# Kernel tuning notes

Measured on AMD Instinct MI355X. Metric: run time of the kernel, lower is better.

The kernel has to match this reference:

```python
import jax, jax.numpy as jnp
import numpy as np

B, N, D, H, HID, EN = 2, 4096, 128, 4, 32, 16
ALPHA = 0.2           # LeakyReLU slope
NEG = -9e15           # masked_fill value from the original code


def setup_inputs() -> dict:
    key = jax.random.key(0)
    ks = jax.random.split(key, 6)
    fea = jax.random.normal(ks[0], (B, N, D), dtype=jnp.float32)
    # binary dense adjacency (regulon x gene), square here so narrow() is identity
    adj = jax.random.randint(ks[1], (B, N, N), 0, 2).astype(jnp.float32)
    # per-head GAT params (xavier-ish scale)
    W_heads = jax.random.normal(ks[2], (H, D, HID), dtype=jnp.float32) * 0.1
    a_heads = jax.random.normal(ks[3], (H, 2 * HID, 1), dtype=jnp.float32) * 0.1
    W_last = jax.random.normal(ks[4], (H * HID, EN), dtype=jnp.float32) * 0.1
    a_last = jax.random.normal(ks[5], (2 * EN, 1), dtype=jnp.float32) * 0.1
    return {"fea_mats": fea, "adj_mats": adj, "W_heads": W_heads,
            "a_heads": a_heads, "W_last": W_last, "a_last": a_last}


def _gat_layer(x, adj, W, a, concat):
    # x: [N, d_in], adj: [nr, N], W: [d_in, out], a: [2*out, 1]
    out_dim = W.shape[1]
    wh = x @ W                                   # [N, out]
    nr = adj.shape[0]
    wh1 = wh[:nr] @ a[:out_dim]                  # [nr, 1]
    wh2 = wh @ a[out_dim:]                       # [N, 1]
    e = jax.nn.leaky_relu(wh1 + wh2.T, ALPHA)    # [nr, N]
    # _prepare_attentions: mask by adj, weight by adj, fill zeros with -9e15
    att = jnp.where(adj != 0, e * adj, 0.0)
    att = jnp.where(att == 0, NEG, att)
    att = jax.nn.softmax(att, axis=1)
    # the original detaches attention via a numpy roundtrip
    att = jax.lax.stop_gradient(att)
    res = att @ wh                               # [nr, out]
    return jax.nn.elu(res) if concat else res


def reference(fea_mats, adj_mats, W_heads, a_heads, W_last, a_last):
    def per_sample(x, adj):
        # multi-head attention layers (concat=True), vmapped over heads
        heads = jax.vmap(lambda W, a: _gat_layer(x, adj, W, a, True))(W_heads, a_heads)  # [H, N, HID]
        xcat = jnp.transpose(heads, (1, 0, 2)).reshape(x.shape[0], H * HID)  # torch.cat(dim=1)
        nr = adj.shape[0]
        out = _gat_layer(xcat, adj[:, :nr], W_last, a_last, False)  # adj.narrow(1,0,nr)
        return jax.nn.elu(out)  # [N, EN]
    return jax.vmap(per_sample)(fea_mats, adj_mats)  # [B, N, EN]
```

## Files before the change

### kernel.cpp

```cpp
#include <hip/hip_runtime.h>
#include <hip/hip_bf16.h>
#include <stdint.h>

#define B_ 2
#define N_ 4096
#define D_ 128
#define H_ 4
#define HID_ 32
#define EN_ 16
#define ALPHA_ 0.2f

typedef __attribute__((ext_vector_type(8))) short bf16x8;
typedef __attribute__((ext_vector_type(4))) float f32x4;
typedef __attribute__((ext_vector_type(8))) unsigned short u16x8;

__device__ __forceinline__ float bf2f(unsigned short u) {
    return __uint_as_float(((unsigned int)u) << 16);
}
__device__ __forceinline__ unsigned short f2bf_rne(float x) {
    unsigned int u = __float_as_uint(x);
    unsigned int r = ((u >> 16) & 1u) + 0x7fffu;
    return (unsigned short)((u + r) >> 16);
}
__device__ __forceinline__ unsigned int f2key(float x) {
    unsigned int u = __float_as_uint(x);
    return (u & 0x80000000u) ? ~u : (u | 0x80000000u);
}
__device__ __forceinline__ float key2f(unsigned int k) {
    unsigned int u = (k & 0x80000000u) ? (k ^ 0x80000000u) : ~k;
    return __uint_as_float(u);
}

__global__ __launch_bounds__(64) void zero_kernel(unsigned int* mk) {
    if (threadIdx.x < 16) mk[threadIdx.x] = 0u;
}

__global__ __launch_bounds__(256) void proj1_kernel(
    const float* __restrict__ fea, const float* __restrict__ Wh,
    float* __restrict__ wh)
{
    __shared__ float Ws[D_ * HID_];
    __shared__ float xs[8][D_];
    const int b = blockIdx.z, h = blockIdx.y;
    const int i0 = blockIdx.x * 8;
    const int tid = threadIdx.x;
    const float* Wp = Wh + h * D_ * HID_;
    for (int idx = tid * 4; idx < D_ * HID_; idx += 1024)
        *(float4*)&Ws[idx] = *(const float4*)(Wp + idx);
    const float* xp = fea + ((size_t)b * N_ + i0) * D_;
    *(float4*)&xs[(tid * 4) >> 7][(tid * 4) & 127] = *(const float4*)(xp + tid * 4);
    __syncthreads();
    const int r = tid >> 5, d = tid & 31;
    float acc = 0.f;
#pragma unroll 8
    for (int k = 0; k < D_; ++k) acc += xs[r][k] * Ws[k * HID_ + d];
    wh[(((size_t)b * H_ + h) * N_ + i0 + r) * HID_ + d] = acc;
}

__global__ __launch_bounds__(128) void proj1b_kernel(
    const float* __restrict__ wh, const float* __restrict__ a_heads,
    float* __restrict__ wh1, float* __restrict__ wh2,
    unsigned int* __restrict__ mkey, unsigned short* __restrict__ whTt)
{
    __shared__ float as_[2 * HID_];
    __shared__ unsigned short ts[32][136];
    const int b = blockIdx.z, h = blockIdx.y, tid = threadIdx.x;
    const int i = blockIdx.x * 128 + tid;
    if (tid < 2 * HID_) as_[tid] = a_heads[h * 2 * HID_ + tid];
    __syncthreads();
    const float* row = wh + (((size_t)b * H_ + h) * N_ + i) * HID_;
    float rv[32];
#pragma unroll
    for (int q = 0; q < 8; ++q) *(float4*)&rv[q * 4] = ((const float4*)row)[q];
    float a1 = 0.f, a2 = 0.f;
#pragma unroll
    for (int d = 0; d < HID_; ++d) {
        float v = rv[d];
        a1 += v * as_[d]; a2 += v * as_[HID_ + d];
        ts[d][tid] = f2bf_rne(v);
    }
    const size_t o = (size_t)(b * H_ + h) * N_ + i;
    wh1[o] = a1; wh2[o] = a2;
    float m = a2;
#pragma unroll
    for (int off = 32; off; off >>= 1) m = fmaxf(m, __shfl_xor(m, off));
    if ((tid & 63) == 0) atomicMax(&mkey[b * H_ + h], f2key(m));
    __syncthreads();
    const size_t base = ((size_t)(b * H_ + h) * 64 + blockIdx.x * 2) * 2048;
#pragma unroll
    for (int r = 0; r < 4; ++r) {
        int l = r * 128 + tid;
        int jb = l >> 8, d = (l >> 3) & 31, part = l & 7;
        *(u16x8*)(whTt + base + (size_t)jb * 2048 + d * 64 + part * 8) =
            *(const u16x8*)&ts[d][jb * 64 + part * 8];
    }
}

__global__ __launch_bounds__(256) void attn1_kernel(
    const float* __restrict__ adj, const unsigned short* __restrict__ whT,
    const float* __restrict__ wh1, const float* __restrict__ wh2,
    const unsigned int* __restrict__ mkey, float* __restrict__ x2)
{
    __shared__ float adj_s[2][16][68];
    __shared__ unsigned short whT_s[2][4][32][72];
    __shared__ float wh2_s[2][H_][64];
    __shared__ float lred[4][16];
    const int b = blockIdx.y, i0 = blockIdx.x * 16;
    const int tid = threadIdx.x, lane = tid & 63, h = tid >> 6;
    const int m = lane & 15, quad = lane >> 4;
    const float w1r = wh1[(size_t)(b * H_ + h) * N_ + i0 + m];
    const float Mh = key2f(mkey[b * H_ + h]);
    const float sb = w1r + Mh;
    const float mr = sb > 0.f ? sb : ALPHA_ * sb;
    const float* adjb = adj + ((size_t)b * N_ + i0) * N_;
    const float* wh2h = wh2 + (size_t)(b * H_ + h) * N_;
    const unsigned short* whTh = whT + (size_t)(b * H_ + h) * 64 * 2048;
    f32x4 acc0 = {0.f, 0.f, 0.f, 0.f}, acc1 = {0.f, 0.f, 0.f, 0.f};
    float lsum = 0.f;
    const int sr = tid >> 4, sc4 = (tid & 15) * 4;

    auto stage = [&](int jt, int buf) {
        *(float4*)&adj_s[buf][sr][sc4] = *(const float4*)(adjb + (size_t)sr * N_ + jt + sc4);
        wh2_s[buf][h][lane] = wh2h[jt + lane];
        const unsigned short* src = whTh + ((size_t)(jt >> 6)) * 2048;
#pragma unroll
        for (int r = 0; r < 4; ++r) {
            int l = r * 64 + lane;
            int d = l >> 3, part = l & 7;
            *(u16x8*)&whT_s[buf][h][d][part * 8] = *(const u16x8*)(src + l * 8);
        }
    };
    auto compute = [&](int buf) {
#pragma unroll
        for (int ks = 0; ks < 2; ++ks) {
            const int ko = ks * 32 + quad * 8;
            float a[8], w[8];
            *(float4*)&a[0] = *(const float4*)&adj_s[buf][m][ko];
            *(float4*)&a[4] = *(const float4*)&adj_s[buf][m][ko + 4];
            *(float4*)&w[0] = *(const float4*)&wh2_s[buf][h][ko];
            *(float4*)&w[4] = *(const float4*)&wh2_s[buf][h][ko + 4];
            bf16x8 af;
#pragma unroll
            for (int jj = 0; jj < 8; ++jj) {
                float s = w1r + w[jj];
                float e = s > 0.f ? s : ALPHA_ * s;
                float sc = e * a[jj];
                float p = (a[jj] != 0.f && sc != 0.f) ? __expf(sc - mr) : 0.f;
                unsigned short pb = f2bf_rne(p);
                af[jj] = (short)pb;
                lsum += bf2f(pb);
            }
            bf16x8 b0 = *(const bf16x8*)&whT_s[buf][h][m][ko];
            bf16x8 b1 = *(const bf16x8*)&whT_s[buf][h][m + 16][ko];
            acc0 = __builtin_amdgcn_mfma_f32_16x16x32_bf16(af, b0, acc0, 0, 0, 0);
            acc1 = __builtin_amdgcn_mfma_f32_16x16x32_bf16(af, b1, acc1, 0, 0, 0);
        }
    };

    stage(0, 0);
    int buf = 0;
    for (int jt = 0; jt < N_; jt += 64) {
        __syncthreads();
        if (jt + 64 < N_) stage(jt + 64, buf ^ 1);
        compute(buf);
        buf ^= 1;
    }
    lsum += __shfl_xor(lsum, 16);
    lsum += __shfl_xor(lsum, 32);
    if (lane < 16) lred[h][lane] = lsum;
    __syncthreads();
    float* obase = x2 + ((size_t)b * N_ + i0) * (H_ * HID_) + h * HID_;
#pragma unroll
    for (int reg = 0; reg < 4; ++reg) {
        int row = quad * 4 + reg;
        float linv = 1.f / fmaxf(lred[h][row], 1e-30f);
        float v0 = acc0[reg] * linv;
        float v1 = acc1[reg] * linv;
        v0 = v0 > 0.f ? v0 : expm1f(v0);
        v1 = v1 > 0.f ? v1 : expm1f(v1);
        obase[(size_t)row * (H_ * HID_) + m] = v0;
        obase[(size_t)row * (H_ * HID_) + 16 + m] = v1;
    }
}

__global__ __launch_bounds__(256) void proj2_kernel(
    const float* __restrict__ x2, const float* __restrict__ Wl,
    float* __restrict__ whl2)
{
    __shared__ float Ws[D_ * EN_];
    __shared__ float xs[16][D_];
    const int b = blockIdx.y, i0 = blockIdx.x * 16, tid = threadIdx.x;
    for (int idx = tid * 4; idx < D_ * EN_; idx += 1024)
        *(float4*)&Ws[idx] = *(const float4*)(Wl + idx);
    const float* xp = x2 + ((size_t)b * N_ + i0) * D_;
    for (int idx = tid * 4; idx < 16 * D_; idx += 1024)
        *(float4*)&xs[idx >> 7][idx & 127] = *(const float4*)(xp + idx);
    __syncthreads();
    const int r = tid >> 4, e = tid & 15;
    float acc = 0.f;
#pragma unroll 8
    for (int k = 0; k < D_; ++k) acc += xs[r][k] * Ws[k * EN_ + e];
    whl2[((size_t)b * N_ + i0 + r) * EN_ + e] = acc;
}

__global__ __launch_bounds__(128) void proj2b_kernel(
    const float* __restrict__ whl2, const float* __restrict__ a_last,
    float* __restrict__ wh1b, float* __restrict__ wh2b,
    unsigned int* __restrict__ mkey2, unsigned short* __restrict__ whT2t)
{
    __shared__ float as_[2 * EN_];
    __shared__ unsigned short ts[16][136];
    const int b = blockIdx.y, tid = threadIdx.x;
    const int i = blockIdx.x * 128 + tid;
    if (tid < 2 * EN_) as_[tid] = a_last[tid];
    __syncthreads();
    const float* row = whl2 + ((size_t)b * N_ + i) * EN_;
    float rv[16];
#pragma unroll
    for (int q = 0; q < 4; ++q) *(float4*)&rv[q * 4] = ((const float4*)row)[q];
    float a1 = 0.f, a2 = 0.f;
#pragma unroll
    for (int e = 0; e < EN_; ++e) {
        float v = rv[e];
        a1 += v * as_[e]; a2 += v * as_[EN_ + e];
        ts[e][tid] = f2bf_rne(v);
    }
    wh1b[(size_t)b * N_ + i] = a1; wh2b[(size_t)b * N_ + i] = a2;
    float m = a2;
#pragma unroll
    for (int off = 32; off; off >>= 1) m = fmaxf(m, __shfl_xor(m, off));
    if ((tid & 63) == 0) atomicMax(mkey2 + b, f2key(m));
    __syncthreads();
    const size_t base = ((size_t)b * 64 + blockIdx.x * 2) * 1024;
#pragma unroll
    for (int r = 0; r < 2; ++r) {
        int l = r * 128 + tid;
        int jb = l >> 7, d = (l >> 3) & 15, part = l & 7;
        *(u16x8*)(whT2t + base + (size_t)jb * 1024 + d * 64 + part * 8) =
            *(const u16x8*)&ts[d][jb * 64 + part * 8];
    }
}

__global__ __launch_bounds__(256) void attn2_kernel(
    const float* __restrict__ adj, const unsigned short* __restrict__ whT2,
    const float* __restrict__ wh1b, const float* __restrict__ wh2b,
    const unsigned int* __restrict__ mkey2, float* __restrict__ out)
{
    __shared__ float adj_s[2][16][268];
    __shared__ unsigned short wT_s[2][16][264];
    __shared__ float w2_s[2][256];
    __shared__ float accred[4][16][17];
    __shared__ float lredp[4][16];
    const int b = blockIdx.y, i0 = blockIdx.x * 16;
    const int tid = threadIdx.x, lane = tid & 63, w = tid >> 6;
    const int m = lane & 15, quad = lane >> 4;
    const float w1r = wh1b[(size_t)b * N_ + i0 + m];
    const float Mh = key2f(mkey2[b]);
    const float sb = w1r + Mh;
    const float mr = sb > 0.f ? sb : ALPHA_ * sb;
    const float* adjb = adj + ((size_t)b * N_ + i0) * N_;
    const float* w2g = wh2b + (size_t)b * N_;
    const unsigned short* wTg = whT2 + (size_t)b * 64 * 1024;
    f32x4 acc = {0.f, 0.f, 0.f, 0.f};
    float lsum = 0.f;
    const int sr = tid >> 4, sc = (tid & 15) * 4;

    auto stage = [&](int jt, int buf) {
#pragma unroll
        for (int r = 0; r < 4; ++r)
            *(float4*)&adj_s[buf][sr][r * 64 + sc] =
                *(const float4*)(adjb + (size_t)sr * N_ + jt + r * 64 + sc);
        w2_s[buf][tid] = w2g[jt + tid];
#pragma unroll
        for (int r = 0; r < 2; ++r) {
            int l = r * 256 + tid;
            int jb = l >> 7, t = l & 127;
            int d = t >> 3, part = t & 7;
            *(u16x8*)&wT_s[buf][d][jb * 64 + part * 8] =
                *(const u16x8*)(wTg + ((size_t)(jt >> 6) + jb) * 1024 + d * 64 + part * 8);
        }
    };
    auto compute = [&](int buf) {
#pragma unroll
        for (int ks = 0; ks < 2; ++ks) {
            const int ko = w * 64 + ks * 32 + quad * 8;
            float a[8], ww[8];
            *(float4*)&a[0] = *(const float4*)&adj_s[buf][m][ko];
            *(float4*)&a[4] = *(const float4*)&adj_s[buf][m][ko + 4];
            *(float4*)&ww[0] = *(const float4*)&w2_s[buf][ko];
            *(float4*)&ww[4] = *(const float4*)&w2_s[buf][ko + 4];
            bf16x8 af;
#pragma unroll
            for (int jj = 0; jj < 8; ++jj) {
                float s = w1r + ww[jj];
                float e = s > 0.f ? s : ALPHA_ * s;
                float sc2 = e * a[jj];
                float p = (a[jj] != 0.f && sc2 != 0.f) ? __expf(sc2 - mr) : 0.f;
                unsigned short pb = f2bf_rne(p);
                af[jj] = (short)pb;
                lsum += bf2f(pb);
            }
            bf16x8 bfr = *(const bf16x8*)&wT_s[buf][m][ko];
            acc = __builtin_amdgcn_mfma_f32_16x16x32_bf16(af, bfr, acc, 0, 0, 0);
        }
    };

    stage(0, 0);
    int buf = 0;
    for (int jt = 0; jt < N_; jt += 256) {
        __syncthreads();
        if (jt + 256 < N_) stage(jt + 256, buf ^ 1);
        compute(buf);
        buf ^= 1;
    }
    lsum += __shfl_xor(lsum, 16);
    lsum += __shfl_xor(lsum, 32);
    if (lane < 16) lredp[w][lane] = lsum;
#pragma unroll
    for (int reg = 0; reg < 4; ++reg)
        accred[w][quad * 4 + reg][m] = acc[reg];
    __syncthreads();
    const int row = tid >> 4, col = tid & 15;
    float s = accred[0][row][col] + accred[1][row][col]
            + accred[2][row][col] + accred[3][row][col];
    float l = lredp[0][row] + lredp[1][row] + lredp[2][row] + lredp[3][row];
    float v = s / fmaxf(l, 1e-30f);
    out[((size_t)b * N_ + i0 + row) * EN_ + col] = v > 0.f ? v : expm1f(v);
}

extern "C" void kernel_launch(void* const* d_in, const int* in_sizes, int n_in,
                              void* d_out, int out_size, void* d_ws, size_t ws_size,
                              hipStream_t stream)
{
    const float* fea = (const float*)d_in[0];
    const float* adj = (const float*)d_in[1];
    const float* Wh  = (const float*)d_in[2];
    const float* ah  = (const float*)d_in[3];
    const float* Wl  = (const float*)d_in[4];
    const float* al  = (const float*)d_in[5];

    float* ws   = (float*)d_ws;
    float* wh   = ws;
    float* wh1  = wh  + (size_t)B_ * H_ * N_ * HID_;
    float* wh2  = wh1 + (size_t)B_ * H_ * N_;
    float* x2   = wh2 + (size_t)B_ * H_ * N_;
    float* whl2 = x2  + (size_t)B_ * N_ * D_;
    float* wh1b = whl2 + (size_t)B_ * N_ * EN_;
    float* wh2b = wh1b + (size_t)B_ * N_;
    unsigned int* mkey = (unsigned int*)(wh2b + (size_t)B_ * N_);
    unsigned short* whTt  = (unsigned short*)(mkey + 16);
    unsigned short* whT2t = whTt + (size_t)B_ * H_ * 64 * 2048;

    zero_kernel<<<1, 64, 0, stream>>>(mkey);
    proj1_kernel<<<dim3(N_ / 8, H_, B_), 256, 0, stream>>>(fea, Wh, wh);
    proj1b_kernel<<<dim3(N_ / 128, H_, B_), 128, 0, stream>>>(wh, ah, wh1, wh2, mkey, whTt);
    attn1_kernel<<<dim3(N_ / 16, B_), 256, 0, stream>>>(adj, whTt, wh1, wh2, mkey, x2);
    proj2_kernel<<<dim3(N_ / 16, B_), 256, 0, stream>>>(x2, Wl, whl2);
    proj2b_kernel<<<dim3(N_ / 128, B_), 128, 0, stream>>>(whl2, al, wh1b, wh2b, mkey + 8, whT2t);
    attn2_kernel<<<dim3(N_ / 16, B_), 256, 0, stream>>>(adj, whT2t, wh1b, wh2b, mkey + 8,
                                                        (float*)d_out);
}
```

Baseline: 341.6 us.

## Split attention over key dimension with atomic accumulation and fused heads

Both attention kernels now split the key (j) dimension across S blocks and accumulate partial numerators and softmax denominators with float atomics. The normalisation and ELU are deferred to proj2 and a new finalize kernel. attn1 now processes all four heads per wave, reading the adjacency row once instead of staging it through shared memory. The exponent is moved to exp2 by pre-scaling the logits with log2(e). The change removes LDS double-buffering, adds a memset and many atomics, and makes results order-nondeterministic. It also changes the masking semantics slightly: sc!=0 becomes s!=0, and e*adj is treated as e for binary adjacency.

```diff
diff --git a/kernel.cpp b/kernel.cpp
--- a/kernel.cpp
+++ b/kernel.cpp
@@ -9,6 +9,9 @@
 #define HID_ 32
 #define EN_ 16
 #define ALPHA_ 0.2f
+#define S1_ 8
+#define S2_ 8
+#define LOG2E_ 1.4426950408889634f
 
 typedef __attribute__((ext_vector_type(8))) short bf16x8;
 typedef __attribute__((ext_vector_type(4))) float f32x4;
@@ -29,10 +32,6 @@
 __device__ __forceinline__ float key2f(unsigned int k) {
     unsigned int u = (k & 0x80000000u) ? (k ^ 0x80000000u) : ~k;
     return __uint_as_float(u);
-}
-
-__global__ __launch_bounds__(64) void zero_kernel(unsigned int* mk) {
-    if (threadIdx.x < 16) mk[threadIdx.x] = 0u;
 }
 
 __global__ __launch_bounds__(256) void proj1_kernel(
@@ -79,6 +78,7 @@
         a1 += v * as_[d]; a2 += v * as_[HID_ + d];
         ts[d][tid] = f2bf_rne(v);
     }
+    a1 *= LOG2E_; a2 *= LOG2E_;
     const size_t o = (size_t)(b * H_ + h) * N_ + i;
     wh1[o] = a1; wh2[o] = a2;
     float m = a2;
@@ -99,102 +99,106 @@
 __global__ __launch_bounds__(256) void attn1_kernel(
     const float* __restrict__ adj, const unsigned short* __restrict__ whT,
     const float* __restrict__ wh1, const float* __restrict__ wh2,
-    const unsigned int* __restrict__ mkey, float* __restrict__ x2)
-{
-    __shared__ float adj_s[2][16][68];
-    __shared__ unsigned short whT_s[2][4][32][72];
-    __shared__ float wh2_s[2][H_][64];
-    __shared__ float lred[4][16];
-    const int b = blockIdx.y, i0 = blockIdx.x * 16;
-    const int tid = threadIdx.x, lane = tid & 63, h = tid >> 6;
+    const unsigned int* __restrict__ mkey,
+    float* __restrict__ x2num, float* __restrict__ l1sum)
+{
+    const int b = blockIdx.z, split = blockIdx.y;
+    const int tid = threadIdx.x, lane = tid & 63, wv = tid >> 6;
+    const int i0 = blockIdx.x * 64 + wv * 16;
     const int m = lane & 15, quad = lane >> 4;
-    const float w1r = wh1[(size_t)(b * H_ + h) * N_ + i0 + m];
-    const float Mh = key2f(mkey[b * H_ + h]);
-    const float sb = w1r + Mh;
-    const float mr = sb > 0.f ? sb : ALPHA_ * sb;
-    const float* adjb = adj + ((size_t)b * N_ + i0) * N_;
-    const float* wh2h = wh2 + (size_t)(b * H_ + h) * N_;
-    const unsigned short* whTh = whT + (size_t)(b * H_ + h) * 64 * 2048;
-    f32x4 acc0 = {0.f, 0.f, 0.f, 0.f}, acc1 = {0.f, 0.f, 0.f, 0.f};
-    float lsum = 0.f;
-    const int sr = tid >> 4, sc4 = (tid & 15) * 4;
-
-    auto stage = [&](int jt, int buf) {
-        *(float4*)&adj_s[buf][sr][sc4] = *(const float4*)(adjb + (size_t)sr * N_ + jt + sc4);
-        wh2_s[buf][h][lane] = wh2h[jt + lane];
-        const unsigned short* src = whTh + ((size_t)(jt >> 6)) * 2048;
-#pragma unroll
-        for (int r = 0; r < 4; ++r) {
-            int l = r * 64 + lane;
-            int d = l >> 3, part = l & 7;
-            *(u16x8*)&whT_s[buf][h][d][part * 8] = *(const u16x8*)(src + l * 8);
+    const int jb0 = split * (N_ / S1_ / 64);
+    float w1r[H_], mr[H_];
+    const float* w2h[H_];
+    const unsigned short* whTp[H_];
+#pragma unroll
+    for (int h = 0; h < H_; ++h) {
+        w1r[h] = wh1[(size_t)(b * H_ + h) * N_ + i0 + m];
+        float Mh = key2f(mkey[b * H_ + h]);
+        float sb = w1r[h] + Mh;
+        mr[h] = fmaxf(sb, ALPHA_ * sb);
+        w2h[h] = wh2 + (size_t)(b * H_ + h) * N_;
+        whTp[h] = whT + (size_t)(b * H_ + h) * 64 * 2048;
+    }
+    const float* adjr = adj + ((size_t)b * N_ + i0 + m) * N_;
+    f32x4 acc0[H_], acc1[H_];
+    float lsum[H_];
+#pragma unroll
+    for (int h = 0; h < H_; ++h) {
+        acc0[h] = (f32x4){0.f, 0.f, 0.f, 0.f};
+        acc1[h] = (f32x4){0.f, 0.f, 0.f, 0.f};
+        lsum[h] = 0.f;
+    }
+
+    for (int t = 0; t < N_ / S1_ / 64; ++t) {
+        const int jb = jb0 + t;
+#pragma unroll
+        for (int ks = 0; ks < 2; ++ks) {
+            const int jo = (jb << 6) + ks * 32 + quad * 8;
+            float av[8];
+            *(float4*)&av[0] = *(const float4*)(adjr + jo);
+            *(float4*)&av[4] = *(const float4*)(adjr + jo + 4);
+#pragma unroll
+            for (int h = 0; h < H_; ++h) {
+                float wv8[8];
+                *(float4*)&wv8[0] = *(const float4*)(w2h[h] + jo);
+                *(float4*)&wv8[4] = *(const float4*)(w2h[h] + jo + 4);
+                bf16x8 af;
+#pragma unroll
+                for (int jj = 0; jj < 8; ++jj) {
+                    float s = w1r[h] + wv8[jj];
+                    float e = fmaxf(s, ALPHA_ * s);
+                    float tt = (av[jj] == 0.f || s == 0.f) ? -__builtin_inff()
+                                                           : (e - mr[h]);
+                    float p = __builtin_amdgcn_exp2f(tt);
+                    unsigned short pb = f2bf_rne(p);
+                    af[jj] = (short)pb;
+                    lsum[h] += bf2f(pb);
+                }
+                const unsigned short* bp =
+                    whTp[h] + (size_t)jb * 2048 + m * 64 + ks * 32 + quad * 8;
+                bf16x8 b0 = *(const bf16x8*)bp;
+                bf16x8 b1 = *(const bf16x8*)(bp + 1024);
+                acc0[h] = __builtin_amdgcn_mfma_f32_16x16x32_bf16(af, b0, acc0[h], 0, 0, 0);
+                acc1[h] = __builtin_amdgcn_mfma_f32_16x16x32_bf16(af, b1, acc1[h], 0, 0, 0);
+            }
         }
-    };
-    auto compute = [&](int buf) {
-#pragma unroll
-        for (int ks = 0; ks < 2; ++ks) {
-            const int ko = ks * 32 + quad * 8;
-            float a[8], w[8];
-            *(float4*)&a[0] = *(const float4*)&adj_s[buf][m][ko];
-            *(float4*)&a[4] = *(const float4*)&adj_s[buf][m][ko + 4];
-            *(float4*)&w[0] = *(const float4*)&wh2_s[buf][h][ko];
-            *(float4*)&w[4] = *(const float4*)&wh2_s[buf][h][ko + 4];
-            bf16x8 af;
-#pragma unroll
-            for (int jj = 0; jj < 8; ++jj) {
-                float s = w1r + w[jj];
-                float e = s > 0.f ? s : ALPHA_ * s;
-                float sc = e * a[jj];
-                float p = (a[jj] != 0.f && sc != 0.f) ? __expf(sc - mr) : 0.f;
-                unsigned short pb = f2bf_rne(p);
-                af[jj] = (short)pb;
-                lsum += bf2f(pb);
-            }
-            bf16x8 b0 = *(const bf16x8*)&whT_s[buf][h][m][ko];
-            bf16x8 b1 = *(const bf16x8*)&whT_s[buf][h][m + 16][ko];
-            acc0 = __builtin_amdgcn_mfma_f32_16x16x32_bf16(af, b0, acc0, 0, 0, 0);
-            acc1 = __builtin_amdgcn_mfma_f32_16x16x32_bf16(af, b1, acc1, 0, 0, 0);
+    }
+#pragma unroll
+    for (int h = 0; h < H_; ++h) {
+#pragma unroll
+        for (int reg = 0; reg < 4; ++reg) {
+            int row = quad * 4 + reg;
+            float* dst = x2num + ((size_t)b * N_ + i0 + row) * (H_ * HID_) + h * HID_;
+            atomicAdd(dst + m, acc0[h][reg]);
+            atomicAdd(dst + 16 + m, acc1[h][reg]);
         }
-    };
-
-    stage(0, 0);
-    int buf = 0;
-    for (int jt = 0; jt < N_; jt += 64) {
-        __syncthreads();
-        if (jt + 64 < N_) stage(jt + 64, buf ^ 1);
-        compute(buf);
-        buf ^= 1;
-    }
-    lsum += __shfl_xor(lsum, 16);
-    lsum += __shfl_xor(lsum, 32);
-    if (lane < 16) lred[h][lane] = lsum;
-    __syncthreads();
-    float* obase = x2 + ((size_t)b * N_ + i0) * (H_ * HID_) + h * HID_;
-#pragma unroll
-    for (int reg = 0; reg < 4; ++reg) {
-        int row = quad * 4 + reg;
-        float linv = 1.f / fmaxf(lred[h][row], 1e-30f);
-        float v0 = acc0[reg] * linv;
-        float v1 = acc1[reg] * linv;
-        v0 = v0 > 0.f ? v0 : expm1f(v0);
-        v1 = v1 > 0.f ? v1 : expm1f(v1);
-        obase[(size_t)row * (H_ * HID_) + m] = v0;
-        obase[(size_t)row * (H_ * HID_) + 16 + m] = v1;
-    }
+        lsum[h] += __shfl_xor(lsum[h], 16);
+        lsum[h] += __shfl_xor(lsum[h], 32);
+    }
+    float lv = quad == 0 ? lsum[0] : quad == 1 ? lsum[1] : quad == 2 ? lsum[2] : lsum[3];
+    atomicAdd(l1sum + ((size_t)b * N_ + i0 + m) * H_ + quad, lv);
 }
 
 __global__ __launch_bounds__(256) void proj2_kernel(
-    const float* __restrict__ x2, const float* __restrict__ Wl,
-    float* __restrict__ whl2)
+    const float* __restrict__ x2num, const float* __restrict__ l1sum,
+    const float* __restrict__ Wl, float* __restrict__ whl2)
 {
     __shared__ float Ws[D_ * EN_];
     __shared__ float xs[16][D_];
     const int b = blockIdx.y, i0 = blockIdx.x * 16, tid = threadIdx.x;
     for (int idx = tid * 4; idx < D_ * EN_; idx += 1024)
         *(float4*)&Ws[idx] = *(const float4*)(Wl + idx);
-    const float* xp = x2 + ((size_t)b * N_ + i0) * D_;
-    for (int idx = tid * 4; idx < 16 * D_; idx += 1024)
-        *(float4*)&xs[idx >> 7][idx & 127] = *(const float4*)(xp + idx);
+    for (int idx = tid * 4; idx < 16 * D_; idx += 1024) {
+        int r = idx >> 7, hd = idx & 127, h = hd >> 5;
+        const size_t i = (size_t)b * N_ + i0 + r;
+        float linv = 1.f / fmaxf(l1sum[i * H_ + h], 1e-30f);
+        float4 v = *(const float4*)(x2num + i * D_ + hd);
+        float o0 = v.x * linv, o1 = v.y * linv, o2 = v.z * linv, o3 = v.w * linv;
+        xs[r][hd]     = o0 > 0.f ? o0 : expm1f(o0);
+        xs[r][hd + 1] = o1 > 0.f ? o1 : expm1f(o1);
+        xs[r][hd + 2] = o2 > 0.f ? o2 : expm1f(o2);
+        xs[r][hd + 3] = o3 > 0.f ? o3 : expm1f(o3);
+    }
     __syncthreads();
     const int r = tid >> 4, e = tid & 15;
     float acc = 0.f;
@@ -225,6 +229,7 @@
         a1 += v * as_[e]; a2 += v * as_[EN_ + e];
         ts[e][tid] = f2bf_rne(v);
     }
+    a1 *= LOG2E_; a2 *= LOG2E_;
     wh1b[(size_t)b * N_ + i] = a1; wh2b[(size_t)b * N_ + i] = a2;
     float m = a2;
 #pragma unroll
@@ -244,88 +249,65 @@
 __global__ __launch_bounds__(256) void attn2_kernel(
     const float* __restrict__ adj, const unsigned short* __restrict__ whT2,
     const float* __restrict__ wh1b, const float* __restrict__ wh2b,
-    const unsigned int* __restrict__ mkey2, float* __restrict__ out)
-{
-    __shared__ float adj_s[2][16][268];
-    __shared__ unsigned short wT_s[2][16][264];
-    __shared__ float w2_s[2][256];
-    __shared__ float accred[4][16][17];
-    __shared__ float lredp[4][16];
-    const int b = blockIdx.y, i0 = blockIdx.x * 16;
-    const int tid = threadIdx.x, lane = tid & 63, w = tid >> 6;
+    const unsigned int* __restrict__ mkey2,
+    float* __restrict__ out_num, float* __restrict__ out_l)
+{
+    const int b = blockIdx.z, split = blockIdx.y;
+    const int tid = threadIdx.x, lane = tid & 63, wv = tid >> 6;
+    const int i0 = blockIdx.x * 64 + wv * 16;
     const int m = lane & 15, quad = lane >> 4;
+    const int jb0 = split * (N_ / S2_ / 64);
     const float w1r = wh1b[(size_t)b * N_ + i0 + m];
     const float Mh = key2f(mkey2[b]);
     const float sb = w1r + Mh;
-    const float mr = sb > 0.f ? sb : ALPHA_ * sb;
-    const float* adjb = adj + ((size_t)b * N_ + i0) * N_;
+    const float mr = fmaxf(sb, ALPHA_ * sb);
+    const float* adjr = adj + ((size_t)b * N_ + i0 + m) * N_;
     const float* w2g = wh2b + (size_t)b * N_;
     const unsigned short* wTg = whT2 + (size_t)b * 64 * 1024;
     f32x4 acc = {0.f, 0.f, 0.f, 0.f};
     float lsum = 0.f;
-    const int sr = tid >> 4, sc = (tid & 15) * 4;
-
-    auto stage = [&](int jt, int buf) {
-#pragma unroll
-        for (int r = 0; r < 4; ++r)
-            *(float4*)&adj_s[buf][sr][r * 64 + sc] =
-                *(const float4*)(adjb + (size_t)sr * N_ + jt + r * 64 + sc);
-        w2_s[buf][tid] = w2g[jt + tid];
-#pragma unroll
-        for (int r = 0; r < 2; ++r) {
-            int l = r * 256 + tid;
-            int jb = l >> 7, t = l & 127;
-            int d = t >> 3, part = t & 7;
-            *(u16x8*)&wT_s[buf][d][jb * 64 + part * 8] =
-                *(const u16x8*)(wTg + ((size_t)(jt >> 6) + jb) * 1024 + d * 64 + part * 8);
-        }
-    };
-    auto compute = [&](int buf) {
+
+    for (int t = 0; t < N_ / S2_ / 64; ++t) {
+        const int jb = jb0 + t;
 #pragma unroll
         for (int ks = 0; ks < 2; ++ks) {
-            const int ko = w * 64 + ks * 32 + quad * 8;
-            float a[8], ww[8];
-            *(float4*)&a[0] = *(const float4*)&adj_s[buf][m][ko];
-            *(float4*)&a[4] = *(const float4*)&adj_s[buf][m][ko + 4];
-            *(float4*)&ww[0] = *(const float4*)&w2_s[buf][ko];
-            *(float4*)&ww[4] = *(const float4*)&w2_s[buf][ko + 4];
+            const int jo = (jb << 6) + ks * 32 + quad * 8;
+            float av[8], wv8[8];
+            *(float4*)&av[0] = *(const float4*)(adjr + jo);
+            *(float4*)&av[4] = *(const float4*)(adjr + jo + 4);
+            *(float4*)&wv8[0] = *(const float4*)(w2g + jo);
+            *(float4*)&wv8[4] = *(const float4*)(w2g + jo + 4);
             bf16x8 af;
 #pragma unroll
             for (int jj = 0; jj < 8; ++jj) {
-                float s = w1r + ww[jj];
-                float e = s > 0.f ? s : ALPHA_ * s;
-                float sc2 = e * a[jj];
-                float p = (a[jj] != 0.f && sc2 != 0.f) ? __expf(sc2 - mr) : 0.f;
+                float s = w1r + wv8[jj];
+                float e = fmaxf(s, ALPHA_ * s);
+                float tt = (av[jj] == 0.f || s == 0.f) ? -__builtin_inff() : (e - mr);
+                float p = __builtin_amdgcn_exp2f(tt);
                 unsigned short pb = f2bf_rne(p);
                 af[jj] = (short)pb;
                 lsum += bf2f(pb);
             }
-            bf16x8 bfr = *(const bf16x8*)&wT_s[buf][m][ko];
-            acc = __builtin_amdgcn_mfma_f32_16x16x32_bf16(af, bfr, acc, 0, 0, 0);
+            bf16x8 b0 = *(const bf16x8*)(wTg + (size_t)jb * 1024 + m * 64 + ks * 32 + quad * 8);
+            acc = __builtin_amdgcn_mfma_f32_16x16x32_bf16(af, b0, acc, 0, 0, 0);
         }
-    };
-
-    stage(0, 0);
-    int buf = 0;
-    for (int jt = 0; jt < N_; jt += 256) {
-        __syncthreads();
-        if (jt + 256 < N_) stage(jt + 256, buf ^ 1);
-        compute(buf);
-        buf ^= 1;
+    }
+#pragma unroll
+    for (int reg = 0; reg < 4; ++reg) {
+        int row = quad * 4 + reg;
+        atomicAdd(out_num + ((size_t)b * N_ + i0 + row) * EN_ + m, acc[reg]);
     }
     lsum += __shfl_xor(lsum, 16);
     lsum += __shfl_xor(lsum, 32);
-    if (lane < 16) lredp[w][lane] = lsum;
-#pragma unroll
-    for (int reg = 0; reg < 4; ++reg)
-        accred[w][quad * 4 + reg][m] = acc[reg];
-    __syncthreads();
-    const int row = tid >> 4, col = tid & 15;
-    float s = accred[0][row][col] + accred[1][row][col]
-            + accred[2][row][col] + accred[3][row][col];
-    float l = lredp[0][row] + lredp[1][row] + lredp[2][row] + lredp[3][row];
-    float v = s / fmaxf(l, 1e-30f);
-    out[((size_t)b * N_ + i0 + row) * EN_ + col] = v > 0.f ? v : expm1f(v);
+    if (quad == 0) atomicAdd(out_l + (size_t)b * N_ + i0 + m, lsum);
+}
+
+__global__ __launch_bounds__(256) void finalize2_kernel(
+    const float* __restrict__ num, const float* __restrict__ l, float* __restrict__ out)
+{
+    const int id = blockIdx.x * 256 + threadIdx.x;
+    float v = num[id] / fmaxf(l[id >> 4], 1e-30f);
+    out[id] = v > 0.f ? v : expm1f(v);
 }
 
 extern "C" void kernel_launch(void* const* d_in, const int* in_sizes, int n_in,
@@ -339,24 +321,30 @@
     const float* Wl  = (const float*)d_in[4];
     const float* al  = (const float*)d_in[5];
 
-    float* ws   = (float*)d_ws;
-    float* wh   = ws;
-    float* wh1  = wh  + (size_t)B_ * H_ * N_ * HID_;
-    float* wh2  = wh1 + (size_t)B_ * H_ * N_;
-    float* x2   = wh2 + (size_t)B_ * H_ * N_;
-    float* whl2 = x2  + (size_t)B_ * N_ * D_;
-    float* wh1b = whl2 + (size_t)B_ * N_ * EN_;
-    float* wh2b = wh1b + (size_t)B_ * N_;
-    unsigned int* mkey = (unsigned int*)(wh2b + (size_t)B_ * N_);
+    float* ws    = (float*)d_ws;
+    float* wh    = ws;
+    float* wh1   = wh   + (size_t)B_ * H_ * N_ * HID_;
+    float* wh2   = wh1  + (size_t)B_ * H_ * N_;
+    float* whl2  = wh2  + (size_t)B_ * H_ * N_;
+    float* wh1b  = whl2 + (size_t)B_ * N_ * EN_;
+    float* wh2b  = wh1b + (size_t)B_ * N_;
+    float* x2num  = wh2b + (size_t)B_ * N_;
+    float* l1sum  = x2num + (size_t)B_ * N_ * D_;
+    float* outnum = l1sum + (size_t)B_ * N_ * H_;
+    float* outl   = outnum + (size_t)B_ * N_ * EN_;
+    unsigned int* mkey = (unsigned int*)(outl + (size_t)B_ * N_);
+    size_t zero_bytes = ((size_t)B_ * N_ * (D_ + H_ + EN_ + 1)) * 4 + 64;
     unsigned short* whTt  = (unsigned short*)(mkey + 16);
     unsigned short* whT2t = whTt + (size_t)B_ * H_ * 64 * 2048;
 
-    zero_kernel<<<1, 64, 0, stream>>>(mkey);
+    hipMemsetAsync(x2num, 0, zero_bytes, stream);
     proj1_kernel<<<dim3(N_ / 8, H_, B_), 256, 0, stream>>>(fea, Wh, wh);
     proj1b_kernel<<<dim3(N_ / 128, H_, B_), 128, 0, stream>>>(wh, ah, wh1, wh2, mkey, whTt);
-    attn1_kernel<<<dim3(N_ / 16, B_), 256, 0, stream>>>(adj, whTt, wh1, wh2, mkey, x2);
-    proj2_kernel<<<dim3(N_ / 16, B_), 256, 0, stream>>>(x2, Wl, whl2);
+    attn1_kernel<<<dim3(N_ / 64, S1_, B_), 256, 0, stream>>>(adj, whTt, wh1, wh2, mkey,
+                                                             x2num, l1sum);
+    proj2_kernel<<<dim3(N_ / 16, B_), 256, 0, stream>>>(x2num, l1sum, Wl, whl2);
     proj2b_kernel<<<dim3(N_ / 128, B_), 128, 0, stream>>>(whl2, al, wh1b, wh2b, mkey + 8, whT2t);
-    attn2_kernel<<<dim3(N_ / 16, B_), 256, 0, stream>>>(adj, whT2t, wh1b, wh2b, mkey + 8,
-                                                        (float*)d_out);
-}
+    attn2_kernel<<<dim3(N_ / 64, S2_, B_), 256, 0, stream>>>(adj, whT2t, wh1b, wh2b, mkey + 8,
+                                                             outnum, outl);
+    finalize2_kernel<<<(B_ * N_ * EN_) / 256, 256, 0, stream>>>(outnum, outl, (float*)d_out);
+}
```

Result: slower. 373.7 us (+9.4%).
